# Optimization experiments

Measured on AMD Instinct MI355X. Metric: run time of the kernel, lower is better.

The kernel has to match this reference:

```python
import jax, jax.numpy as jnp
import numpy as np

N = 50000
E = 800000
IN_C = 128
HID = 16
HEADS = 8
OUT_C = 64
NEG_SLOPE = 0.2


def setup_inputs() -> dict:
    key = jax.random.key(0)
    ks = jax.random.split(key, 12)
    x = jax.random.normal(ks[0], (N, IN_C), dtype=jnp.float32)
    edge_index = jax.random.randint(ks[1], (2, E), 0, N, dtype=jnp.int32)
    s = 0.1
    W1 = jax.random.normal(ks[2], (IN_C, HEADS * HID), dtype=jnp.float32) * s
    a1_src = jax.random.normal(ks[3], (HEADS, HID), dtype=jnp.float32) * s
    a1_dst = jax.random.normal(ks[4], (HEADS, HID), dtype=jnp.float32) * s
    b1 = jnp.zeros((HEADS * HID,), dtype=jnp.float32)
    W2 = jax.random.normal(ks[5], (HEADS * HID, OUT_C), dtype=jnp.float32) * s
    a2_src = jax.random.normal(ks[6], (1, OUT_C), dtype=jnp.float32) * s
    a2_dst = jax.random.normal(ks[7], (1, OUT_C), dtype=jnp.float32) * s
    b2 = jnp.zeros((OUT_C,), dtype=jnp.float32)
    return {"x": x, "edge_index": edge_index, "W1": W1, "a1_src": a1_src,
            "a1_dst": a1_dst, "b1": b1, "W2": W2, "a2_src": a2_src,
            "a2_dst": a2_dst, "b2": b2}


def gat_conv(x, src, dst, W, a_src, a_dst, b, heads, ch):
    # linear projection -> [N, H, C]
    h = (x @ W).reshape(N, heads, ch)
    # per-node attention logits [N, H]
    al_s = jnp.einsum('nhc,hc->nh', h, a_src)
    al_d = jnp.einsum('nhc,hc->nh', h, a_dst)
    # per-edge logits [E, H]
    e = jax.nn.leaky_relu(al_s[src] + al_d[dst], NEG_SLOPE)
    # segment softmax over incoming edges of each dst node
    emax = jax.ops.segment_max(e, dst, num_segments=N)
    ee = jnp.exp(e - emax[dst])
    denom = jax.ops.segment_sum(ee, dst, num_segments=N)
    alpha = ee / (denom[dst] + 1e-16)
    # weighted scatter-aggregate of source messages
    msg = h[src] * alpha[:, :, None]  # [E, H, C]
    out = jax.ops.segment_sum(msg, dst, num_segments=N)
    return out.reshape(N, heads * ch) + b


def reference(x, edge_index, W1, a1_src, a1_dst, b1, W2, a2_src, a2_dst, b2):
    # add self loops (PyG GATConv default add_self_loops=True)
    loops = jnp.arange(N, dtype=edge_index.dtype)
    src = jnp.concatenate([edge_index[0], loops])
    dst = jnp.concatenate([edge_index[1], loops])
    h = gat_conv(x, src, dst, W1, a1_src, a1_dst, b1, HEADS, HID)
    h = jax.nn.relu(h)
    # dropout p=0.6 is identity in eval mode
    out = gat_conv(h, src, dst, W2, a2_src, a2_dst, b2, 1, OUT_C)
    return out
```

## Files before the change

### kernel.cpp

```cpp
#include <hip/hip_runtime.h>
#include <hip/hip_fp16.h>
#include <math.h>

#define N_NODES 50000
#define E_EDGES 800000
#define IN_C    128
#define HID     16
#define HEADS   8
#define OUT_C   64
#define NEG_SLOPE 0.2f
#define CELLW   64

#define WCOLS   144
#define WSTRIDE 136
#define WBYTES  (WCOLS * WSTRIDE * 2)

typedef _Float16 half8 __attribute__((ext_vector_type(8)));
typedef _Float16 half4 __attribute__((ext_vector_type(4)));
typedef float floatx4 __attribute__((ext_vector_type(4)));

__device__ __forceinline__ float lrelu_exp(float v) {
    v = v > 0.f ? v : NEG_SLOPE * v;
    return __expf(v);
}

__device__ __forceinline__ void gload_lds16(const void* g, void* l) {
    __builtin_amdgcn_global_load_lds(
        (const __attribute__((address_space(1))) void*)g,
        (__attribute__((address_space(3))) void*)l, 16, 0, 0);
}

__global__ __launch_bounds__(256) void prep(
    const float* __restrict__ W1, const float* __restrict__ a1_src,
    const float* __restrict__ a1_dst, _Float16* __restrict__ W1t,
    int* __restrict__ cursor) {
    const int t = threadIdx.x;
    const int n = blockIdx.x * 256 + t;
    if (n < N_NODES) cursor[n] = 0;
    if (blockIdx.x == 0) {
        const int col = t & 127;
        const int kq = (t >> 7) * 4;
        for (int it = 0; it < 16; ++it) {
            const int k0 = it * 8 + kq;
            half4 hv;
            hv[0] = (_Float16)W1[(size_t)(k0 + 0) * IN_C + col];
            hv[1] = (_Float16)W1[(size_t)(k0 + 1) * IN_C + col];
            hv[2] = (_Float16)W1[(size_t)(k0 + 2) * IN_C + col];
            hv[3] = (_Float16)W1[(size_t)(k0 + 3) * IN_C + col];
            *(half4*)&W1t[col * WSTRIDE + k0] = hv;
        }
    } else if (blockIdx.x == 1) {
        const int j = t & 15;
        const int k0 = (t >> 4) * 8;
        const float* av = (j < 8) ? (a1_src + j * 16) : (a1_dst + (j - 8) * 16);
        const int hc = (j & 7) * 16;
        for (int k = k0; k < k0 + 8; ++k) {
            float s = 0.f;
#pragma unroll
            for (int c = 0; c < 16; ++c) s += W1[(size_t)k * IN_C + hc + c] * av[c];
            W1t[(128 + j) * WSTRIDE + k] = (_Float16)s;
        }
    }
}

__global__ __launch_bounds__(512, 6) void fused_gemm_fill(
    const float* __restrict__ X, const _Float16* __restrict__ W1t,
    __half* __restrict__ H,
    float* __restrict__ als, float* __restrict__ ald,
    const int* __restrict__ src, const int* __restrict__ dst,
    int* __restrict__ cursor, int* __restrict__ ell) {
    __shared__ _Float16 wT[WCOLS * WSTRIDE];
    const int bid = blockIdx.x;
    const int t = threadIdx.x;

    {
        const char* g = (const char*)W1t;
        char* l = (char*)wT;
        const int o = t * 16;
#pragma unroll
        for (int it = 0; it < 4; ++it) {
            const int off = it * 8192 + o;
            gload_lds16(g + off, l + off);
        }
        if (t < 400) {
            const int off = 32768 + o;
            gload_lds16(g + off, l + off);
        }
    }

    const int wave = t >> 6, lane = t & 63;
    const int m = lane & 15, quad = lane >> 4;

    const float* Xr = nullptr;
    int r0w = 0;
    float4 xv0, xv1, xv2, xv3;
    if (wave < 4) {
        r0w = bid * 64 + wave * 16;
        int rl = r0w + m;
        if (rl >= N_NODES) rl = N_NODES - 1;
        Xr = X + (size_t)rl * IN_C;
        const int q8 = quad * 8;
        xv0 = *(const float4*)(Xr + q8);
        xv1 = *(const float4*)(Xr + q8 + 4);
        xv2 = *(const float4*)(Xr + 32 + q8);
        xv3 = *(const float4*)(Xr + 32 + q8 + 4);
    }

    __syncthreads();

    if (wave >= 4) {
        const int tid = bid * 256 + (t - 256);
        if (tid < E_EDGES / 4) {
            const int4 s4 = ((const int4*)src)[tid];
            const int4 d4 = ((const int4*)dst)[tid];
            const int p0 = atomicAdd(&cursor[d4.x], 1);
            const int p1 = atomicAdd(&cursor[d4.y], 1);
            const int p2 = atomicAdd(&cursor[d4.z], 1);
            const int p3 = atomicAdd(&cursor[d4.w], 1);
            if (p0 < CELLW) __builtin_nontemporal_store(s4.x, &ell[(size_t)d4.x * CELLW + p0]);
            if (p1 < CELLW) __builtin_nontemporal_store(s4.y, &ell[(size_t)d4.y * CELLW + p1]);
            if (p2 < CELLW) __builtin_nontemporal_store(s4.z, &ell[(size_t)d4.z * CELLW + p2]);
            if (p3 < CELLW) __builtin_nontemporal_store(s4.w, &ell[(size_t)d4.w * CELLW + p3]);
        }
        return;
    }

    floatx4 acc[9];
#pragma unroll
    for (int i = 0; i < 9; ++i) acc[i] = (floatx4){0.f, 0.f, 0.f, 0.f};

#pragma unroll
    for (int kc = 0; kc < 4; ++kc) {
        const int k8 = kc * 32 + quad * 8;
        float4 xa, xb;
        if (kc == 0)      { xa = xv0; xb = xv1; }
        else if (kc == 1) { xa = xv2; xb = xv3; }
        else {
            xa = *(const float4*)(Xr + k8);
            xb = *(const float4*)(Xr + k8 + 4);
        }
        half8 a;
        a[0] = (_Float16)xa.x; a[1] = (_Float16)xa.y;
        a[2] = (_Float16)xa.z; a[3] = (_Float16)xa.w;
        a[4] = (_Float16)xb.x; a[5] = (_Float16)xb.y;
        a[6] = (_Float16)xb.z; a[7] = (_Float16)xb.w;
#pragma unroll
        for (int ct = 0; ct < 9; ++ct) {
            const half8 b = *(const half8*)&wT[(ct * 16 + m) * WSTRIDE + k8];
            acc[ct] = __builtin_amdgcn_mfma_f32_16x16x32_f16(a, b, acc[ct], 0, 0, 0);
        }
    }

    _Float16* Hh = (_Float16*)H;
#pragma unroll
    for (int ct = 0; ct < 8; ++ct) {
#pragma unroll
        for (int r = 0; r < 4; ++r) {
            const int row = r0w + quad * 4 + r;
            if (row < N_NODES)
                Hh[(size_t)row * IN_C + ct * 16 + m] = (_Float16)acc[ct][r];
        }
    }
#pragma unroll
    for (int r = 0; r < 4; ++r) {
        const int row = r0w + quad * 4 + r;
        if (row < N_NODES) {
            if (m < 8) als[(size_t)row * HEADS + m] = acc[8][r];
            else       ald[(size_t)row * HEADS + (m - 8)] = acc[8][r];
        }
    }
}

__global__ __launch_bounds__(256) void agg1_gemm2(
    const int* __restrict__ cnt, const int* __restrict__ ell,
    const float* __restrict__ als, const float* __restrict__ ald,
    const __half* __restrict__ H, const float* __restrict__ b,
    const float* __restrict__ W2, const float* __restrict__ a2_src,
    const float* __restrict__ a2_dst, __half* __restrict__ H2,
    float* __restrict__ als2, float* __restrict__ ald2) {
    __shared__ _Float16 w2T[OUT_C * 136];
    __shared__ _Float16 xrowh[32 * 136];
    __shared__ float l2buf[2][32][2];
    const int t = threadIdx.x;

    {
        const int col = t & 63;
        const int kg = t >> 6;
        for (int k0 = kg * 32; k0 < kg * 32 + 32; k0 += 4) {
            half4 hv;
            hv[0] = (_Float16)W2[(size_t)(k0 + 0) * OUT_C + col];
            hv[1] = (_Float16)W2[(size_t)(k0 + 1) * OUT_C + col];
            hv[2] = (_Float16)W2[(size_t)(k0 + 2) * OUT_C + col];
            hv[3] = (_Float16)W2[(size_t)(k0 + 3) * OUT_C + col];
            *(half4*)&w2T[col * 136 + k0] = hv;
        }
    }

    const int nl = t >> 3, h = t & 7;
    int nc = blockIdx.x * 32 + nl;
    if (nc >= N_NODES) nc = N_NODES - 1;
    int deg = cnt[nc];
    deg = deg < CELLW ? deg : CELLW;
    const int* ep = ell + (size_t)nc * CELLW;
    const float ad = ald[nc * HEADS + h];
    float accv[16];
    float ssum;
    {
        const float w = lrelu_exp(als[nc * HEADS + h] + ad);
        const half8* q = (const half8*)(H + ((size_t)nc * HEADS + h) * HID);
        const half8 u0 = q[0], u1 = q[1];
        ssum = w;
#pragma unroll
        for (int j = 0; j < 8; ++j) {
            accv[j] = w * (float)u0[j];
            accv[j + 8] = w * (float)u1[j];
        }
    }
    for (int p = 0; p < deg; p += 4) {
        const int4 s4 = *(const int4*)(ep + p);
        const int s0 = s4.x;
        const int i1 = (p + 1 < deg) ? s4.y : nc;
        const int i2 = (p + 2 < deg) ? s4.z : nc;
        const int i3 = (p + 3 < deg) ? s4.w : nc;
        const float f1 = (p + 1 < deg) ? 1.f : 0.f;
        const float f2 = (p + 2 < deg) ? 1.f : 0.f;
        const float f3 = (p + 3 < deg) ? 1.f : 0.f;
        const float v0 = als[s0 * HEADS + h];
        const float v1 = als[i1 * HEADS + h];
        const float v2 = als[i2 * HEADS + h];
        const float v3 = als[i3 * HEADS + h];
        const half8* q0 = (const half8*)(H + ((size_t)s0 * HEADS + h) * HID);
        const half8* q1 = (const half8*)(H + ((size_t)i1 * HEADS + h) * HID);
        const half8* q2 = (const half8*)(H + ((size_t)i2 * HEADS + h) * HID);
        const half8* q3 = (const half8*)(H + ((size_t)i3 * HEADS + h) * HID);
        const half8 a0 = q0[0], b0 = q0[1];
        const half8 a1 = q1[0], b1 = q1[1];
        const half8 a2 = q2[0], b2 = q2[1];
        const half8 a3 = q3[0], b3 = q3[1];
        const float w0 = lrelu_exp(v0 + ad);
        const float w1 = lrelu_exp(v1 + ad) * f1;
        const float w2 = lrelu_exp(v2 + ad) * f2;
        const float w3 = lrelu_exp(v3 + ad) * f3;
        ssum += (w0 + w1) + (w2 + w3);
#pragma unroll
        for (int j = 0; j < 8; ++j) {
            accv[j]     += w0 * (float)a0[j] + w1 * (float)a1[j] +
                           w2 * (float)a2[j] + w3 * (float)a3[j];
            accv[j + 8] += w0 * (float)b0[j] + w1 * (float)b1[j] +
                           w2 * (float)b2[j] + w3 * (float)b3[j];
        }
    }
    {
        const float inv = 1.f / (ssum + 1e-16f);
        half8 r0, r1;
#pragma unroll
        for (int j = 0; j < 8; ++j) {
            float ra = accv[j] * inv + b[h * 16 + j];
            float rb = accv[j + 8] * inv + b[h * 16 + 8 + j];
            r0[j] = (_Float16)(ra > 0.f ? ra : 0.f);
            r1[j] = (_Float16)(rb > 0.f ? rb : 0.f);
        }
        _Float16* xr = &xrowh[nl * 136 + h * 16];
        *(half8*)(xr) = r0;
        *(half8*)(xr + 8) = r1;
    }

    __syncthreads();

    {
        const int wv = t >> 6, ln = t & 63;
        const int bm = ln & 15, quad = ln >> 4;
        const int mt = wv >> 1;
        const int ntg = wv & 1;
        floatx4 acc0 = (floatx4){0.f, 0.f, 0.f, 0.f};
        floatx4 acc1 = (floatx4){0.f, 0.f, 0.f, 0.f};
        const _Float16* arow  = &xrowh[(mt * 16 + bm) * 136];
        const _Float16* brow0 = &w2T[(ntg * 32 + bm) * 136];
        const _Float16* brow1 = &w2T[(ntg * 32 + 16 + bm) * 136];
#pragma unroll
        for (int kc = 0; kc < 4; ++kc) {
            const int k8 = kc * 32 + quad * 8;
            const half8 a   = *(const half8*)(arow + k8);
            const half8 b0v = *(const half8*)(brow0 + k8);
            const half8 b1v = *(const half8*)(brow1 + k8);
            acc0 = __builtin_amdgcn_mfma_f32_16x16x32_f16(a, b0v, acc0, 0, 0, 0);
            acc1 = __builtin_amdgcn_mfma_f32_16x16x32_f16(a, b1v, acc1, 0, 0, 0);
        }
        const float a2s0 = a2_src[ntg * 32 + bm],      a2d0 = a2_dst[ntg * 32 + bm];
        const float a2s1 = a2_src[ntg * 32 + 16 + bm], a2d1 = a2_dst[ntg * 32 + 16 + bm];
        _Float16* H2h = (_Float16*)H2;
        float psr[4], pdr[4];
#pragma unroll
        for (int r = 0; r < 4; ++r) {
            const float c0 = acc0[r], c1 = acc1[r];
            float ps = c0 * a2s0 + c1 * a2s1;
            float pd = c0 * a2d0 + c1 * a2d1;
            ps += __shfl_xor(ps, 1); pd += __shfl_xor(pd, 1);
            ps += __shfl_xor(ps, 2); pd += __shfl_xor(pd, 2);
            ps += __shfl_xor(ps, 4); pd += __shfl_xor(pd, 4);
            ps += __shfl_xor(ps, 8); pd += __shfl_xor(pd, 8);
            psr[r] = ps; pdr[r] = pd;
            const int row = blockIdx.x * 32 + mt * 16 + quad * 4 + r;
            if (row < N_NODES) {
                H2h[(size_t)row * OUT_C + ntg * 32 + bm] = (_Float16)c0;
                H2h[(size_t)row * OUT_C + ntg * 32 + 16 + bm] = (_Float16)c1;
            }
        }
        if (bm == 0) {
#pragma unroll
            for (int r = 0; r < 4; ++r) {
                l2buf[ntg][mt * 16 + quad * 4 + r][0] = psr[r];
                l2buf[ntg][mt * 16 + quad * 4 + r][1] = pdr[r];
            }
        }
    }
    __syncthreads();
    if (t < 32) {
        const int n2 = blockIdx.x * 32 + t;
        if (n2 < N_NODES) {
            als2[n2] = l2buf[0][t][0] + l2buf[1][t][0];
            ald2[n2] = l2buf[0][t][1] + l2buf[1][t][1];
        }
    }
}

__global__ __launch_bounds__(256) void agg2(
    const int* __restrict__ cnt, const int* __restrict__ ell,
    const float* __restrict__ als, const float* __restrict__ ald,
    const __half* __restrict__ H, const float* __restrict__ b,
    float* __restrict__ out) {
    const int t = threadIdx.x;
    int n = blockIdx.x * 32 + (t >> 3);
    const int j0 = (t & 7) * 8;
    const bool valid = n < N_NODES;
    if (!valid) n = N_NODES - 1;
    int deg = cnt[n];
    deg = deg < CELLW ? deg : CELLW;
    const int* ep = ell + (size_t)n * CELLW;
    const float ad = ald[n];
    float accv[8];
    float ssum;
    {
        const float w = lrelu_exp(als[n] + ad);
        const half8 u = *(const half8*)(H + (size_t)n * OUT_C + j0);
        ssum = w;
#pragma unroll
        for (int k = 0; k < 8; ++k) accv[k] = w * (float)u[k];
    }
    for (int p = 0; p < deg; p += 4) {
        const int4 s4 = *(const int4*)(ep + p);
        const int s0 = s4.x;
        const int i1 = (p + 1 < deg) ? s4.y : n;
        const int i2 = (p + 2 < deg) ? s4.z : n;
        const int i3 = (p + 3 < deg) ? s4.w : n;
        const float f1 = (p + 1 < deg) ? 1.f : 0.f;
        const float f2 = (p + 2 < deg) ? 1.f : 0.f;
        const float f3 = (p + 3 < deg) ? 1.f : 0.f;
        const float v0 = als[s0];
        const float v1 = als[i1];
        const float v2 = als[i2];
        const float v3 = als[i3];
        const half8 u0 = *(const half8*)(H + (size_t)s0 * OUT_C + j0);
        const half8 u1 = *(const half8*)(H + (size_t)i1 * OUT_C + j0);
        const half8 u2 = *(const half8*)(H + (size_t)i2 * OUT_C + j0);
        const half8 u3 = *(const half8*)(H + (size_t)i3 * OUT_C + j0);
        const float w0 = lrelu_exp(v0 + ad);
        const float w1 = lrelu_exp(v1 + ad) * f1;
        const float w2 = lrelu_exp(v2 + ad) * f2;
        const float w3 = lrelu_exp(v3 + ad) * f3;
        ssum += (w0 + w1) + (w2 + w3);
#pragma unroll
        for (int k = 0; k < 8; ++k)
            accv[k] += w0 * (float)u0[k] + w1 * (float)u1[k] +
                       w2 * (float)u2[k] + w3 * (float)u3[k];
    }
    if (valid) {
        const float inv = 1.f / (ssum + 1e-16f);
        floatx4 r0, r1;
        r0[0] = accv[0] * inv + b[j0 + 0]; r0[1] = accv[1] * inv + b[j0 + 1];
        r0[2] = accv[2] * inv + b[j0 + 2]; r0[3] = accv[3] * inv + b[j0 + 3];
        r1[0] = accv[4] * inv + b[j0 + 4]; r1[1] = accv[5] * inv + b[j0 + 5];
        r1[2] = accv[6] * inv + b[j0 + 6]; r1[3] = accv[7] * inv + b[j0 + 7];
        float* op = out + (size_t)n * OUT_C + j0;
        __builtin_nontemporal_store(r0, (floatx4*)op);
        __builtin_nontemporal_store(r1, (floatx4*)(op + 4));
    }
}

extern "C" void kernel_launch(void* const* d_in, const int* in_sizes, int n_in,
                              void* d_out, int out_size, void* d_ws, size_t ws_size,
                              hipStream_t stream) {
    const float* x      = (const float*)d_in[0];
    const int*   ei     = (const int*)d_in[1];
    const float* W1     = (const float*)d_in[2];
    const float* a1_src = (const float*)d_in[3];
    const float* a1_dst = (const float*)d_in[4];
    const float* b1     = (const float*)d_in[5];
    const float* W2     = (const float*)d_in[6];
    const float* a2_src = (const float*)d_in[7];
    const float* a2_dst = (const float*)d_in[8];
    const float* b2     = (const float*)d_in[9];
    const int* src = ei;
    const int* dst = ei + E_EDGES;
    float* outp = (float*)d_out;

    char* wsb = (char*)d_ws;
    __half* h1   = (__half*)wsb;
    __half* h2   = h1 + (size_t)N_NODES * IN_C;
    float*  als1 = (float*)(h2 + (size_t)N_NODES * OUT_C);
    float*  ald1 = als1 + N_NODES * HEADS;
    float*  als2 = ald1 + N_NODES * HEADS;
    float*  ald2 = als2 + N_NODES;
    int*    cursor = (int*)(ald2 + N_NODES);
    int*    ell    = cursor + N_NODES;

    _Float16* W1t = (_Float16*)als2;

    prep<<<(N_NODES + 255) / 256, 256, 0, stream>>>(W1, a1_src, a1_dst, W1t, cursor);

    fused_gemm_fill<<<(N_NODES + 63) / 64, 512, 0, stream>>>(
        x, W1t, h1, als1, ald1, src, dst, cursor, ell);

    agg1_gemm2<<<(N_NODES + 31) / 32, 256, 0, stream>>>(
        cursor, ell, als1, ald1, h1, b1, W2, a2_src, a2_dst, h2, als2, ald2);

    agg2<<<(N_NODES + 31) / 32, 256, 0, stream>>>(
        cursor, ell, als2, ald2, h2, b2, outp);
}
```

Baseline: 210.3 us.

## Split fused GEMM/edge-fill kernel into interleaved specialized 256-thread blocks

The fused kernel used to run 512-thread blocks in which four waves did the X@W1 MFMA GEMM and four waves filled the ELL adjacency with atomics. It now launches twice as many 256-thread blocks: odd blocks only do the edge fill and even blocks only do the GEMM. Fill blocks therefore skip the 39KB LDS weight load and the barrier, and GEMM blocks prefetch all X rows into registers before the sync. The change relies on the scheduler balancing the two kinds of blocks, but it loses the guaranteed co-residency that overlapped atomics with MFMA work. The launch_bounds occupancy hint is also dropped.

```diff
diff --git a/kernel.cpp b/kernel.cpp
--- a/kernel.cpp
+++ b/kernel.cpp
@@ -63,7 +63,7 @@
     }
 }
 
-__global__ __launch_bounds__(512, 6) void fused_gemm_fill(
+__global__ __launch_bounds__(256) void fused_gemm_fill(
     const float* __restrict__ X, const _Float16* __restrict__ W1t,
     __half* __restrict__ H,
     float* __restrict__ als, float* __restrict__ ald,
@@ -73,43 +73,8 @@
     const int bid = blockIdx.x;
     const int t = threadIdx.x;
 
-    {
-        const char* g = (const char*)W1t;
-        char* l = (char*)wT;
-        const int o = t * 16;
-#pragma unroll
-        for (int it = 0; it < 4; ++it) {
-            const int off = it * 8192 + o;
-            gload_lds16(g + off, l + off);
-        }
-        if (t < 400) {
-            const int off = 32768 + o;
-            gload_lds16(g + off, l + off);
-        }
-    }
-
-    const int wave = t >> 6, lane = t & 63;
-    const int m = lane & 15, quad = lane >> 4;
-
-    const float* Xr = nullptr;
-    int r0w = 0;
-    float4 xv0, xv1, xv2, xv3;
-    if (wave < 4) {
-        r0w = bid * 64 + wave * 16;
-        int rl = r0w + m;
-        if (rl >= N_NODES) rl = N_NODES - 1;
-        Xr = X + (size_t)rl * IN_C;
-        const int q8 = quad * 8;
-        xv0 = *(const float4*)(Xr + q8);
-        xv1 = *(const float4*)(Xr + q8 + 4);
-        xv2 = *(const float4*)(Xr + 32 + q8);
-        xv3 = *(const float4*)(Xr + 32 + q8 + 4);
-    }
-
-    __syncthreads();
-
-    if (wave >= 4) {
-        const int tid = bid * 256 + (t - 256);
+    if (bid & 1) {
+        const int tid = (bid >> 1) * 256 + t;
         if (tid < E_EDGES / 4) {
             const int4 s4 = ((const int4*)src)[tid];
             const int4 d4 = ((const int4*)dst)[tid];
@@ -125,20 +90,47 @@
         return;
     }
 
-    floatx4 acc[9];
-#pragma unroll
-    for (int i = 0; i < 9; ++i) acc[i] = (floatx4){0.f, 0.f, 0.f, 0.f};
-
+    {
+        const char* g = (const char*)W1t;
+        char* l = (char*)wT;
+        const int o = t * 16;
+#pragma unroll
+        for (int it = 0; it < 9; ++it) {
+            const int off = it * 4096 + o;
+            gload_lds16(g + off, l + off);
+        }
+        if (t < 144) {
+            const int off = 36864 + o;
+            gload_lds16(g + off, l + off);
+        }
+    }
+
+    const int wave = t >> 6, lane = t & 63;
+    const int m = lane & 15, quad = lane >> 4;
+    const int r0w = (bid >> 1) * 64 + wave * 16;
+    int rl = r0w + m;
+    if (rl >= N_NODES) rl = N_NODES - 1;
+    const float* Xr = X + (size_t)rl * IN_C;
+
+    float4 xv[8];
 #pragma unroll
     for (int kc = 0; kc < 4; ++kc) {
         const int k8 = kc * 32 + quad * 8;
-        float4 xa, xb;
-        if (kc == 0)      { xa = xv0; xb = xv1; }
-        else if (kc == 1) { xa = xv2; xb = xv3; }
-        else {
-            xa = *(const float4*)(Xr + k8);
-            xb = *(const float4*)(Xr + k8 + 4);
-        }
+        xv[kc * 2]     = *(const float4*)(Xr + k8);
+        xv[kc * 2 + 1] = *(const float4*)(Xr + k8 + 4);
+    }
+
+    __syncthreads();
+
+    floatx4 acc[9];
+#pragma unroll
+    for (int i = 0; i < 9; ++i) acc[i] = (floatx4){0.f, 0.f, 0.f, 0.f};
+
+#pragma unroll
+    for (int kc = 0; kc < 4; ++kc) {
+        const int k8 = kc * 32 + quad * 8;
+        const float4 xa = xv[kc * 2];
+        const float4 xb = xv[kc * 2 + 1];
         half8 a;
         a[0] = (_Float16)xa.x; a[1] = (_Float16)xa.y;
         a[2] = (_Float16)xa.z; a[3] = (_Float16)xa.w;
@@ -418,8 +410,11 @@
 
     prep<<<(N_NODES + 255) / 256, 256, 0, stream>>>(W1, a1_src, a1_dst, W1t, cursor);
 
-    fused_gemm_fill<<<(N_NODES + 63) / 64, 512, 0, stream>>>(
-        x, W1t, h1, als1, ald1, src, dst, cursor, ell);
+    {
+        const int gemm_blocks = (N_NODES + 63) / 64;
+        fused_gemm_fill<<<gemm_blocks * 2, 256, 0, stream>>>(
+            x, W1t, h1, als1, ald1, src, dst, cursor, ell);
+    }
 
     agg1_gemm2<<<(N_NODES + 31) / 32, 256, 0, stream>>>(
         cursor, ell, als1, ald1, h1, b1, W2, a2_src, a2_dst, h2, als2, ald2);
```

Result: faster. 190.7 us (-9.3%).
